# Kernel optimization log

Measured on AMD Instinct MI355X. Metric: run time of the kernel, lower is better.

## Reference

```python
import jax, jax.numpy as jnp
import numpy as np
import math

D_MODEL = 1024
NUM_HEADS = 16
D_HEAD = D_MODEL // NUM_HEADS          # 64
N_FREQ = D_HEAD // 2 + 1               # 33 rfft bins
COMPRESSION_RATIO = 0.5


def setup_inputs() -> dict:
    key = jax.random.key(0)
    k_x, k_qkv, k_out, k_b, k_m = jax.random.split(key, 5)
    B, S = 2, 2048
    x = jax.random.normal(k_x, (B, S, D_MODEL), dtype=jnp.float32)
    # Linear weights stored as [in, out] (torch Linear uses [out, in]; math identical).
    w_qkv = jax.random.normal(k_qkv, (D_MODEL, 3 * D_MODEL), dtype=jnp.float32) / math.sqrt(D_MODEL)
    w_out = jax.random.normal(k_out, (D_MODEL, D_MODEL), dtype=jnp.float32) / math.sqrt(D_MODEL)
    b_out = jax.random.normal(k_b, (D_MODEL,), dtype=jnp.float32) * 0.01
    # Learned per-frequency-bin mask logits of AdaptiveFrequencyMask(d_state=d_head).
    # Initialized around logit(compression_ratio) with small noise.
    init_logit = math.log(COMPRESSION_RATIO / (1.0 - COMPRESSION_RATIO))
    mask_logits = init_logit + 0.1 * jax.random.normal(k_m, (N_FREQ,), dtype=jnp.float32)
    return {"x": x, "w_qkv": w_qkv, "w_out": w_out, "b_out": b_out, "mask_logits": mask_logits}


def _spectral_filter(t, mask):
    # rfft over d_head dim, apply learned soft mask, inverse rfft.  t: [B,H,S,dh]
    tf = jnp.fft.rfft(t, axis=-1)          # [B,H,S,N_FREQ] complex
    tf = tf * mask                          # broadcast real mask over bins
    return jnp.fft.irfft(tf, n=t.shape[-1], axis=-1).astype(t.dtype)


def reference(x, w_qkv, w_out, b_out, mask_logits):
    B, S, D = x.shape
    H, dh = NUM_HEADS, D_HEAD
    qkv = x @ w_qkv                                         # [B,S,3D]
    q, k, v = jnp.split(qkv, 3, axis=-1)
    # [B,S,D] -> [B,H,S,dh]
    to_heads = lambda t: t.reshape(B, S, H, dh).transpose(0, 2, 1, 3)
    q, k, v = to_heads(q), to_heads(k), to_heads(v)
    mask = jax.nn.sigmoid(mask_logits)                      # [N_FREQ]
    q = _spectral_filter(q, mask)
    k = _spectral_filter(k, mask)
    scores = jnp.einsum('bhqd,bhkd->bhqk', q, k) / math.sqrt(dh)
    attn = jax.nn.softmax(scores, axis=-1)                  # dropout p=0 (eval)
    out = jnp.einsum('bhqk,bhkd->bhqd', attn, v)
    out = out.transpose(0, 2, 1, 3).reshape(B, S, D)
    return out @ w_out + b_out
```

## Files before the change

### kernel.cpp

```cpp
#include <hip/hip_runtime.h>

#define S_LEN 2048
#define NH    16
#define DH    64
#define DM    1024
#define NQKV  3072

typedef __attribute__((ext_vector_type(8))) __bf16 bf16x8;
typedef __attribute__((ext_vector_type(4))) float  f32x4;
typedef unsigned short ushort_t;

static __device__ __forceinline__ unsigned short bf16b(float f) {
  return __builtin_bit_cast(unsigned short, (__bf16)f);
}

static __device__ __forceinline__ float exp2v(float x) {
  return __builtin_amdgcn_exp2f(x);
}

static __device__ __forceinline__ bf16x8 pack8(float4 f0, float4 f1) {
  uint4 v;
  v.x = ((unsigned)bf16b(f0.y) << 16) | bf16b(f0.x);
  v.y = ((unsigned)bf16b(f0.w) << 16) | bf16b(f0.z);
  v.z = ((unsigned)bf16b(f1.y) << 16) | bf16b(f1.x);
  v.w = ((unsigned)bf16b(f1.w) << 16) | bf16b(f1.z);
  return __builtin_bit_cast(bf16x8, v);
}

static __device__ __forceinline__ void glds16(const void* g, void* l) {
  __builtin_amdgcn_global_load_lds((const __attribute__((address_space(1))) unsigned int*)g,
                                   (__attribute__((address_space(3))) unsigned int*)l, 16, 0, 0);
}

#define OFF_WT  65536ull
#define OFF_WOT 6356992ull
#define OFF_Q   8454144ull
#define OFF_K   16842752ull
#define OFF_V   25231360ull
#define OFF_AO  33619968ull

__global__ __launch_bounds__(256) void k_prep(const float* __restrict__ wqkv,
                                              const float* __restrict__ wout,
                                              const float* __restrict__ x,
                                              const float* __restrict__ logits,
                                              unsigned short* __restrict__ Wt,
                                              unsigned short* __restrict__ Wot,
                                              unsigned short* __restrict__ xb) {
  __shared__ __align__(16) char sbuf[16640];
  int bid = blockIdx.x;
  int t = threadIdx.x;

  if (bid < 256) {
    float* msk = (float*)sbuf;
    float* Kd  = (float*)(sbuf + 144);
    ushort_t (*Fb)[72] = (ushort_t(*)[72])(sbuf + 416);
    if (t < 33) msk[t] = 1.0f / (1.0f + __expf(-logits[t]));
    __syncthreads();
    if (t < 64) {
      float acc = msk[0];
      #pragma unroll
      for (int f = 1; f < 32; ++f) {
        int r = (f * t) & 63;
        acc += 2.0f * msk[f] * __cosf((float)r * (6.28318530717958647692f / 64.0f));
      }
      acc += msk[32] * ((t & 1) ? -1.0f : 1.0f);
      Kd[t] = acc * (1.0f / 64.0f);
    }
    __syncthreads();
    for (int idx = t; idx < 4096; idx += 256) {
      int j = idx >> 6, i = idx & 63;
      Fb[j][i] = bf16b(Kd[(j - i) & 63]);
    }
    __syncthreads();

    int lane = t & 63, w = t >> 6;
    int m16 = lane & 15, quad = lane >> 4;
    int kx = bid >> 5, yy = bid & 31;
    int which = yy >> 4, h = yy & 15;
    int base = which * 1024 + h * 64;

    bf16x8 af0 = *(const bf16x8*)(&Fb[w * 16 + m16][quad * 8]);
    bf16x8 af1 = *(const bf16x8*)(&Fb[w * 16 + m16][32 + quad * 8]);

    f32x4 acc[8] = {};
    #pragma unroll 2
    for (int n = 0; n < 8; ++n) {
      const float* Wg = wqkv + (size_t)(kx * 128 + n * 16 + m16) * NQKV + base + quad * 8;
      float4 a0 = *(const float4*)(Wg);
      float4 a1 = *(const float4*)(Wg + 4);
      float4 b0 = *(const float4*)(Wg + 32);
      float4 b1 = *(const float4*)(Wg + 36);
      acc[n] = __builtin_amdgcn_mfma_f32_16x16x32_bf16(af0, pack8(a0, a1), acc[n], 0, 0, 0);
      acc[n] = __builtin_amdgcn_mfma_f32_16x16x32_bf16(af1, pack8(b0, b1), acc[n], 0, 0, 0);
    }
    float sc = (which == 0) ? 0.18033688011112042f : 1.0f;
    #pragma unroll
    for (int n = 0; n < 8; ++n) {
      #pragma unroll
      for (int r = 0; r < 4; ++r) {
        int j = w * 16 + quad * 4 + r;
        Wt[(size_t)(base + j) * DM + kx * 128 + n * 16 + m16] = bf16b(acc[n][r] * sc);
      }
    }
  } else if (bid < 768) {
    float (*Ts)[65] = (float(*)[65])sbuf;
    int b1 = bid - 256;
    if (b1 < 256) {
      int kt = b1 & 15, nt = b1 >> 4;
      int cb = 2048 + nt * 64, kbase = kt * 64;
      #pragma unroll
      for (int p = 0; p < 16; ++p) {
        int kk = p * 4 + (t >> 6);
        Ts[kk][t & 63] = wqkv[(size_t)(kbase + kk) * NQKV + cb + (t & 63)];
      }
      __syncthreads();
      #pragma unroll
      for (int p = 0; p < 16; ++p) {
        int nn = p * 4 + (t >> 6);
        Wt[(size_t)(cb + nn) * DM + kbase + (t & 63)] = bf16b(Ts[t & 63][nn]);
      }
    } else {
      int b2 = b1 - 256;
      int kt = b2 & 15, nt = b2 >> 4;
      int cb = nt * 64, kbase = kt * 64;
      #pragma unroll
      for (int p = 0; p < 16; ++p) {
        int kk = p * 4 + (t >> 6);
        Ts[kk][t & 63] = wout[(size_t)(kbase + kk) * DM + cb + (t & 63)];
      }
      __syncthreads();
      #pragma unroll
      for (int p = 0; p < 16; ++p) {
        int nn = p * 4 + (t >> 6);
        Wot[(size_t)(cb + nn) * DM + kbase + (t & 63)] = bf16b(Ts[t & 63][nn]);
      }
    }
  } else {
    size_t i = ((size_t)(bid - 768) * 256 + t) * 8;
    const float4* xp = (const float4*)(x + i);
    float4 a = xp[0], b = xp[1];
    uint4 v;
    v.x = ((unsigned)bf16b(a.y) << 16) | bf16b(a.x);
    v.y = ((unsigned)bf16b(a.w) << 16) | bf16b(a.z);
    v.z = ((unsigned)bf16b(b.y) << 16) | bf16b(b.x);
    v.w = ((unsigned)bf16b(b.w) << 16) | bf16b(b.z);
    *(uint4*)(xb + i) = v;
  }
}

__device__ __forceinline__ void gemm_core_async(const unsigned short* __restrict__ A,
                                                const unsigned short* __restrict__ Bw,
                                                int bm, int bn, unsigned short* smem,
                                                f32x4 (&acc)[4][4]) {
  unsigned short* As = smem;
  unsigned short* Bs = smem + 8192;
  int t = threadIdx.x, lane = t & 63, w = t >> 6;
  int m16 = lane & 15, quad = lane >> 4;
  int wr = (w >> 1) * 64, wc = (w & 1) * 64;
  int lr = lane >> 3, lc = lane & 7;
  int gc = lc ^ lr;
  int xr = m16 & 7;
  const unsigned short* Agb = A  + (size_t)(bm * 128) * DM + gc * 8;
  const unsigned short* Bgb = Bw + (size_t)(bn * 128) * DM + gc * 8;

  for (int k0 = 0; k0 < DM; k0 += 64) {
    #pragma unroll
    for (int p = 0; p < 4; ++p) {
      int row = p * 32 + w * 8 + lr;
      glds16(Agb + (size_t)row * DM + k0, As + row * 64 + lc * 8);
      glds16(Bgb + (size_t)row * DM + k0, Bs + row * 64 + lc * 8);
    }
    __syncthreads();
    #pragma unroll
    for (int kk = 0; kk < 2; ++kk) {
      bf16x8 af[4], bfr[4];
      #pragma unroll
      for (int i = 0; i < 4; ++i)
        af[i] = *(const bf16x8*)(As + (wr + i * 16 + m16) * 64 + ((kk * 4 + quad) ^ xr) * 8);
      #pragma unroll
      for (int j = 0; j < 4; ++j)
        bfr[j] = *(const bf16x8*)(Bs + (wc + j * 16 + m16) * 64 + ((kk * 4 + quad) ^ xr) * 8);
      #pragma unroll
      for (int i = 0; i < 4; ++i)
        #pragma unroll
        for (int j = 0; j < 4; ++j)
          acc[i][j] = __builtin_amdgcn_mfma_f32_16x16x32_bf16(af[i], bfr[j], acc[i][j], 0, 0, 0);
    }
    __syncthreads();
  }
}

__global__ __launch_bounds__(256) void k_gemm_qkv(const unsigned short* __restrict__ xb,
                                                  const unsigned short* __restrict__ Bw,
                                                  unsigned short* __restrict__ Qb,
                                                  unsigned short* __restrict__ Kb,
                                                  unsigned short* __restrict__ Vt) {
  __shared__ __align__(16) unsigned short smem[18432];
  f32x4 acc[4][4] = {};
  int bn = blockIdx.x, bm = blockIdx.y;
  gemm_core_async(xb, Bw, bm, bn, smem, acc);

  int t = threadIdx.x, lane = t & 63, w = t >> 6;
  int m16 = lane & 15, quad = lane >> 4;
  int wr = (w >> 1) * 64, wc = (w & 1) * 64;
  int b = bm >> 4, srow = (bm & 15) * 128;
  int which = bn >> 3;
  ushort_t (*Tr)[130] = (ushort_t(*)[130])smem;
  if (which < 2) {
    #pragma unroll
    for (int i = 0; i < 4; ++i)
      #pragma unroll
      for (int j = 0; j < 4; ++j)
        #pragma unroll
        for (int r = 0; r < 4; ++r)
          Tr[wr + i * 16 + quad * 4 + r][wc + j * 16 + m16] = bf16b(acc[i][j][r]);
    __syncthreads();
    int row = t >> 1, half = t & 1;
    int cloc = bn * 128 + half * 64 - which * 1024;
    int h = cloc >> 6;
    unsigned short* dst = (which ? Kb : Qb) +
        ((size_t)(b * 16 + h) * 2048 + srow + row) * 64;
    #pragma unroll
    for (int p = 0; p < 8; ++p)
      *(uint4*)(dst + p * 8) = *(const uint4*)(&Tr[row][half * 64 + p * 8]);
  } else {
    #pragma unroll
    for (int i = 0; i < 4; ++i)
      #pragma unroll
      for (int j = 0; j < 4; ++j)
        #pragma unroll
        for (int r = 0; r < 4; ++r)
          Tr[wc + j * 16 + m16][wr + i * 16 + quad * 4 + r] = bf16b(acc[i][j][r]);
    __syncthreads();
    int dl = t >> 1, half = t & 1;
    int cloc = (bn - 16) * 128 + dl;
    int h = cloc >> 6, d = cloc & 63;
    unsigned short* dst = Vt + ((size_t)(b * 16 + h) * 64 + d) * 2048 + srow + half * 64;
    #pragma unroll
    for (int p = 0; p < 8; ++p)
      *(uint4*)(dst + p * 8) = *(const uint4*)(&Tr[dl][half * 64 + p * 8]);
  }
}

__global__ __launch_bounds__(512, 2) void k_attn(const unsigned short* __restrict__ Qb,
                                                 const unsigned short* __restrict__ Kb,
                                                 const unsigned short* __restrict__ Vt,
                                                 unsigned short* __restrict__ AO) {
  __shared__ __align__(16) unsigned short smem[41984];
  int t = threadIdx.x;
  int w = t >> 6, lane = t & 63;
  int m16 = lane & 15, quad = lane >> 4;
  int bid = blockIdx.x;
  int jj = bid >> 3;
  int bh = ((jj & 3) << 3) + (bid & 7);
  int qbase = (jj >> 2) * 256 + w * 32;

  const unsigned short* QpA = Qb + ((size_t)bh * S_LEN + qbase + m16) * DH + quad * 8;
  const unsigned short* QpB = QpA + 16 * DH;
  bf16x8 aq0A = *(const bf16x8*)(QpA);
  bf16x8 aq1A = *(const bf16x8*)(QpA + 32);
  bf16x8 aq0B = *(const bf16x8*)(QpB);
  bf16x8 aq1B = *(const bf16x8*)(QpB + 32);
  const unsigned short* Kbase = Kb + (size_t)bh * S_LEN * DH;
  const unsigned short* Vbase = Vt + (size_t)bh * DH * S_LEN;

  unsigned short* Pw = smem + 24576 + w * 2176;
  int xr = m16 & 7;

  int trow = t >> 3;
  int tcol = t & 7;
  int gswz = tcol ^ (trow & 7);
  const unsigned short* Kg = Kbase + (size_t)trow * 64 + gswz * 8;
  const unsigned short* Vg = Vbase + (size_t)trow * S_LEN + gswz * 8;
  unsigned short* Kl = smem + trow * 64 + tcol * 8;
  unsigned short* Vl = smem + 12288 + trow * 64 + tcol * 8;

  f32x4 oA[4] = {}, oB[4] = {};
  float lA = 0.f, lB = 0.f;
  f32x4 zero = {0.f, 0.f, 0.f, 0.f};

  glds16(Kg,        Kl);
  glds16(Vg,        Vl);
  glds16(Kg + 4096, Kl + 4096);
  glds16(Vg + 64,   Vl + 4096);

  int buf = 0, slot = 2;
  #pragma unroll 1
  for (int kt = 0; kt < S_LEN / 64; ++kt) {
    if (kt + 1 < S_LEN / 64) asm volatile("s_waitcnt vmcnt(2)" ::: "memory");
    else                     asm volatile("s_waitcnt vmcnt(0)" ::: "memory");
    __builtin_amdgcn_s_barrier();
    __builtin_amdgcn_sched_barrier(0);
    if (kt + 2 < S_LEN / 64) {
      glds16(Kg + (size_t)(kt + 2) * 4096, Kl + slot * 4096);
      glds16(Vg + (kt + 2) * 64,           Vl + slot * 4096);
    }
    unsigned short* Ksh = smem + buf * 4096;
    unsigned short* Vsh = smem + 12288 + buf * 4096;

    f32x4 stA[4], stB[4];
    __builtin_amdgcn_s_setprio(1);
    #pragma unroll
    for (int g = 0; g < 4; ++g) {
      int rk = g * 16 + m16;
      bf16x8 kf0 = *(const bf16x8*)(Ksh + rk * 64 + ((quad ^ xr) * 8));
      bf16x8 kf1 = *(const bf16x8*)(Ksh + rk * 64 + (((4 + quad) ^ xr) * 8));
      stA[g] = __builtin_amdgcn_mfma_f32_16x16x32_bf16(kf0, aq0A, zero, 0, 0, 0);
      stA[g] = __builtin_amdgcn_mfma_f32_16x16x32_bf16(kf1, aq1A, stA[g], 0, 0, 0);
      stB[g] = __builtin_amdgcn_mfma_f32_16x16x32_bf16(kf0, aq0B, zero, 0, 0, 0);
      stB[g] = __builtin_amdgcn_mfma_f32_16x16x32_bf16(kf1, aq1B, stB[g], 0, 0, 0);
    }
    __builtin_amdgcn_s_setprio(0);
    #pragma unroll
    for (int g = 0; g < 4; ++g) {
      float a0 = exp2v(stA[g][0]), a1 = exp2v(stA[g][1]);
      float a2 = exp2v(stA[g][2]), a3 = exp2v(stA[g][3]);
      lA += (a0 + a1) + (a2 + a3);
      uint2 pka;
      pka.x = ((unsigned)bf16b(a1) << 16) | bf16b(a0);
      pka.y = ((unsigned)bf16b(a3) << 16) | bf16b(a2);
      *(uint2*)(Pw + m16 * 68 + g * 16 + quad * 4) = pka;
      float b0 = exp2v(stB[g][0]), b1 = exp2v(stB[g][1]);
      float b2 = exp2v(stB[g][2]), b3 = exp2v(stB[g][3]);
      lB += (b0 + b1) + (b2 + b3);
      uint2 pkb;
      pkb.x = ((unsigned)bf16b(b1) << 16) | bf16b(b0);
      pkb.y = ((unsigned)bf16b(b3) << 16) | bf16b(b2);
      *(uint2*)(Pw + (16 + m16) * 68 + g * 16 + quad * 4) = pkb;
    }
    __builtin_amdgcn_s_setprio(1);
    #pragma unroll
    for (int c = 0; c < 2; ++c) {
      bf16x8 apA = *(const bf16x8*)(Pw + m16 * 68 + c * 32 + quad * 8);
      bf16x8 apB = *(const bf16x8*)(Pw + (16 + m16) * 68 + c * 32 + quad * 8);
      #pragma unroll
      for (int j = 0; j < 4; ++j) {
        int dv = j * 16 + m16;
        bf16x8 bv = *(const bf16x8*)(Vsh + dv * 64 + (((c * 4 + quad) ^ xr) * 8));
        oA[j] = __builtin_amdgcn_mfma_f32_16x16x32_bf16(apA, bv, oA[j], 0, 0, 0);
        oB[j] = __builtin_amdgcn_mfma_f32_16x16x32_bf16(apB, bv, oB[j], 0, 0, 0);
      }
    }
    __builtin_amdgcn_s_setprio(0);
    buf  = (buf  == 2) ? 0 : buf  + 1;
    slot = (slot == 2) ? 0 : slot + 1;
  }

  lA += __shfl_xor(lA, 16); lA += __shfl_xor(lA, 32);
  lB += __shfl_xor(lB, 16); lB += __shfl_xor(lB, 32);
  float ivA = 1.0f / lA;
  float ivB = 1.0f / lB;
  int b = bh >> 4, h = bh & 15;
  #pragma unroll
  for (int r = 0; r < 4; ++r) {
    float vA = __shfl(ivA, quad * 4 + r);
    float vB = __shfl(ivB, quad * 4 + r);
    size_t row0 = (size_t)b * S_LEN + qbase + quad * 4 + r;
    unsigned short* d0 = AO + row0 * DM + h * DH + m16;
    unsigned short* d1 = AO + (row0 + 16) * DM + h * DH + m16;
    #pragma unroll
    for (int j = 0; j < 4; ++j) {
      d0[j * 16] = bf16b(oA[j][r] * vA);
      d1[j * 16] = bf16b(oB[j][r] * vB);
    }
  }
}

__global__ __launch_bounds__(256) void k_gemm_out(const unsigned short* __restrict__ A,
                                                  const unsigned short* __restrict__ Bw,
                                                  const float* __restrict__ bias,
                                                  float* __restrict__ out) {
  __shared__ __align__(16) unsigned short smem[18432];
  f32x4 acc[4][4] = {};
  int bn = blockIdx.x, bm = blockIdx.y;
  gemm_core_async(A, Bw, bm, bn, smem, acc);

  int t = threadIdx.x, lane = t & 63, w = t >> 6;
  int m16 = lane & 15, quad = lane >> 4;
  int wr = (w >> 1) * 64, wc = (w & 1) * 64;
  #pragma unroll
  for (int i = 0; i < 4; ++i) {
    int grow = bm * 128 + wr + i * 16 + quad * 4;
    #pragma unroll
    for (int j = 0; j < 4; ++j) {
      int gc = bn * 128 + wc + j * 16 + m16;
      float bb = bias[gc];
      #pragma unroll
      for (int r = 0; r < 4; ++r)
        out[(size_t)(grow + r) * DM + gc] = acc[i][j][r] + bb;
    }
  }
}

extern "C" void kernel_launch(void* const* d_in, const int* in_sizes, int n_in,
                              void* d_out, int out_size, void* d_ws, size_t ws_size,
                              hipStream_t stream) {
  const float* x    = (const float*)d_in[0];
  const float* wqkv = (const float*)d_in[1];
  const float* wout = (const float*)d_in[2];
  const float* bout = (const float*)d_in[3];
  const float* mlog = (const float*)d_in[4];
  char* ws = (char*)d_ws;
  unsigned short* Wt  = (unsigned short*)(ws + OFF_WT);
  unsigned short* Wot = (unsigned short*)(ws + OFF_WOT);
  unsigned short* Qb  = (unsigned short*)(ws + OFF_Q);
  unsigned short* Kb  = (unsigned short*)(ws + OFF_K);
  unsigned short* Vt  = (unsigned short*)(ws + OFF_V);
  unsigned short* xb  = (unsigned short*)(ws + OFF_AO);
  unsigned short* AO  = (unsigned short*)(ws + OFF_AO);
  float* out = (float*)d_out;

  k_prep<<<dim3(2816), dim3(256), 0, stream>>>(wqkv, wout, x, mlog, Wt, Wot, xb);
  k_gemm_qkv<<<dim3(24, 32), dim3(256), 0, stream>>>(xb, Wt, Qb, Kb, Vt);
  k_attn<<<dim3(256), dim3(512), 0, stream>>>(Qb, Kb, Vt, AO);
  k_gemm_out<<<dim3(8, 32), dim3(256), 0, stream>>>(AO, Wot, bout, out);
}
```

Baseline: 218.8 us.

## Process two KV tiles per window with software-pipelined QK and PV stages

The attention loop now handles 128 keys per iteration as two 64-key tiles. The second tile's QK^T MFMAs are interleaved between the first tile's softmax and PV, and K/V loads are issued two tiles at a time into a four-slot double-buffered LDS ring, with one barrier before each refill. The P staging buffer drops the padded 68-stride layout for an XOR-swizzled 64-stride layout with two P slots per wave, and the setprio hints are removed. LDS per block grows from about 82KB to 128KB, which may limit occupancy to one block per CU despite launch_bounds(512,2).

```diff
diff --git a/kernel.cpp b/kernel.cpp
--- a/kernel.cpp
+++ b/kernel.cpp
@@ -246,7 +246,7 @@
                                                  const unsigned short* __restrict__ Kb,
                                                  const unsigned short* __restrict__ Vt,
                                                  unsigned short* __restrict__ AO) {
-  __shared__ __align__(16) unsigned short smem[41984];
+  __shared__ __align__(16) unsigned short smem[65536];
   int t = threadIdx.x;
   int w = t >> 6, lane = t & 63;
   int m16 = lane & 15, quad = lane >> 4;
@@ -264,8 +264,8 @@
   const unsigned short* Kbase = Kb + (size_t)bh * S_LEN * DH;
   const unsigned short* Vbase = Vt + (size_t)bh * DH * S_LEN;
 
-  unsigned short* Pw = smem + 24576 + w * 2176;
   int xr = m16 & 7;
+  unsigned short* Pw = smem + 32768 + w * 4096;
 
   int trow = t >> 3;
   int tcol = t & 7;
@@ -273,77 +273,122 @@
   const unsigned short* Kg = Kbase + (size_t)trow * 64 + gswz * 8;
   const unsigned short* Vg = Vbase + (size_t)trow * S_LEN + gswz * 8;
   unsigned short* Kl = smem + trow * 64 + tcol * 8;
-  unsigned short* Vl = smem + 12288 + trow * 64 + tcol * 8;
+  unsigned short* Vl = smem + 16384 + trow * 64 + tcol * 8;
 
   f32x4 oA[4] = {}, oB[4] = {};
   float lA = 0.f, lB = 0.f;
   f32x4 zero = {0.f, 0.f, 0.f, 0.f};
 
-  glds16(Kg,        Kl);
-  glds16(Vg,        Vl);
-  glds16(Kg + 4096, Kl + 4096);
-  glds16(Vg + 64,   Vl + 4096);
-
-  int buf = 0, slot = 2;
+  #pragma unroll
+  for (int tt = 0; tt < 4; ++tt) {
+    glds16(Kg + (size_t)tt * 4096, Kl + tt * 4096);
+    glds16(Vg + tt * 64,           Vl + tt * 4096);
+  }
+
   #pragma unroll 1
-  for (int kt = 0; kt < S_LEN / 64; ++kt) {
-    if (kt + 1 < S_LEN / 64) asm volatile("s_waitcnt vmcnt(2)" ::: "memory");
-    else                     asm volatile("s_waitcnt vmcnt(0)" ::: "memory");
+  for (int wnd = 0; wnd < 16; ++wnd) {
+    if (wnd < 15) asm volatile("s_waitcnt vmcnt(4)" ::: "memory");
+    else          asm volatile("s_waitcnt vmcnt(0)" ::: "memory");
     __builtin_amdgcn_s_barrier();
     __builtin_amdgcn_sched_barrier(0);
-    if (kt + 2 < S_LEN / 64) {
-      glds16(Kg + (size_t)(kt + 2) * 4096, Kl + slot * 4096);
-      glds16(Vg + (kt + 2) * 64,           Vl + slot * 4096);
-    }
-    unsigned short* Ksh = smem + buf * 4096;
-    unsigned short* Vsh = smem + 12288 + buf * 4096;
-
-    f32x4 stA[4], stB[4];
-    __builtin_amdgcn_s_setprio(1);
+    int sb = (wnd & 1) << 1;
+    const unsigned short* Ka  = smem + sb * 4096;
+    const unsigned short* Kbs = smem + (sb + 1) * 4096;
+    const unsigned short* Va  = smem + 16384 + sb * 4096;
+    const unsigned short* Vbs = smem + 16384 + (sb + 1) * 4096;
+    unsigned short* Pa = Pw;
+    unsigned short* Pb = Pw + 2048;
+
+    f32x4 saA[4], saB[4];
     #pragma unroll
     for (int g = 0; g < 4; ++g) {
       int rk = g * 16 + m16;
-      bf16x8 kf0 = *(const bf16x8*)(Ksh + rk * 64 + ((quad ^ xr) * 8));
-      bf16x8 kf1 = *(const bf16x8*)(Ksh + rk * 64 + (((4 + quad) ^ xr) * 8));
-      stA[g] = __builtin_amdgcn_mfma_f32_16x16x32_bf16(kf0, aq0A, zero, 0, 0, 0);
-      stA[g] = __builtin_amdgcn_mfma_f32_16x16x32_bf16(kf1, aq1A, stA[g], 0, 0, 0);
-      stB[g] = __builtin_amdgcn_mfma_f32_16x16x32_bf16(kf0, aq0B, zero, 0, 0, 0);
-      stB[g] = __builtin_amdgcn_mfma_f32_16x16x32_bf16(kf1, aq1B, stB[g], 0, 0, 0);
-    }
-    __builtin_amdgcn_s_setprio(0);
+      bf16x8 kf0 = *(const bf16x8*)(Ka + rk * 64 + ((quad ^ xr) * 8));
+      bf16x8 kf1 = *(const bf16x8*)(Ka + rk * 64 + (((4 + quad) ^ xr) * 8));
+      saA[g] = __builtin_amdgcn_mfma_f32_16x16x32_bf16(kf0, aq0A, zero, 0, 0, 0);
+      saA[g] = __builtin_amdgcn_mfma_f32_16x16x32_bf16(kf1, aq1A, saA[g], 0, 0, 0);
+      saB[g] = __builtin_amdgcn_mfma_f32_16x16x32_bf16(kf0, aq0B, zero, 0, 0, 0);
+      saB[g] = __builtin_amdgcn_mfma_f32_16x16x32_bf16(kf1, aq1B, saB[g], 0, 0, 0);
+    }
     #pragma unroll
     for (int g = 0; g < 4; ++g) {
-      float a0 = exp2v(stA[g][0]), a1 = exp2v(stA[g][1]);
-      float a2 = exp2v(stA[g][2]), a3 = exp2v(stA[g][3]);
+      int chw = (((2 * g + (quad >> 1)) ^ xr) << 3) + ((quad & 1) << 2);
+      float a0 = exp2v(saA[g][0]), a1 = exp2v(saA[g][1]);
+      float a2 = exp2v(saA[g][2]), a3 = exp2v(saA[g][3]);
       lA += (a0 + a1) + (a2 + a3);
       uint2 pka;
       pka.x = ((unsigned)bf16b(a1) << 16) | bf16b(a0);
       pka.y = ((unsigned)bf16b(a3) << 16) | bf16b(a2);
-      *(uint2*)(Pw + m16 * 68 + g * 16 + quad * 4) = pka;
-      float b0 = exp2v(stB[g][0]), b1 = exp2v(stB[g][1]);
-      float b2 = exp2v(stB[g][2]), b3 = exp2v(stB[g][3]);
+      *(uint2*)(Pa + m16 * 64 + chw) = pka;
+      float b0 = exp2v(saB[g][0]), b1 = exp2v(saB[g][1]);
+      float b2 = exp2v(saB[g][2]), b3 = exp2v(saB[g][3]);
       lB += (b0 + b1) + (b2 + b3);
       uint2 pkb;
       pkb.x = ((unsigned)bf16b(b1) << 16) | bf16b(b0);
       pkb.y = ((unsigned)bf16b(b3) << 16) | bf16b(b2);
-      *(uint2*)(Pw + (16 + m16) * 68 + g * 16 + quad * 4) = pkb;
-    }
-    __builtin_amdgcn_s_setprio(1);
+      *(uint2*)(Pa + (16 + m16) * 64 + chw) = pkb;
+    }
+    f32x4 sbA[4], sbB[4];
+    #pragma unroll
+    for (int g = 0; g < 4; ++g) {
+      int rk = g * 16 + m16;
+      bf16x8 kf0 = *(const bf16x8*)(Kbs + rk * 64 + ((quad ^ xr) * 8));
+      bf16x8 kf1 = *(const bf16x8*)(Kbs + rk * 64 + (((4 + quad) ^ xr) * 8));
+      sbA[g] = __builtin_amdgcn_mfma_f32_16x16x32_bf16(kf0, aq0A, zero, 0, 0, 0);
+      sbA[g] = __builtin_amdgcn_mfma_f32_16x16x32_bf16(kf1, aq1A, sbA[g], 0, 0, 0);
+      sbB[g] = __builtin_amdgcn_mfma_f32_16x16x32_bf16(kf0, aq0B, zero, 0, 0, 0);
+      sbB[g] = __builtin_amdgcn_mfma_f32_16x16x32_bf16(kf1, aq1B, sbB[g], 0, 0, 0);
+    }
     #pragma unroll
     for (int c = 0; c < 2; ++c) {
-      bf16x8 apA = *(const bf16x8*)(Pw + m16 * 68 + c * 32 + quad * 8);
-      bf16x8 apB = *(const bf16x8*)(Pw + (16 + m16) * 68 + c * 32 + quad * 8);
+      bf16x8 apA = *(const bf16x8*)(Pa + m16 * 64 + (((4 * c + quad) ^ xr) << 3));
+      bf16x8 apB = *(const bf16x8*)(Pa + (16 + m16) * 64 + (((4 * c + quad) ^ xr) << 3));
       #pragma unroll
       for (int j = 0; j < 4; ++j) {
         int dv = j * 16 + m16;
-        bf16x8 bv = *(const bf16x8*)(Vsh + dv * 64 + (((c * 4 + quad) ^ xr) * 8));
+        bf16x8 bv = *(const bf16x8*)(Va + dv * 64 + (((c * 4 + quad) ^ xr) * 8));
         oA[j] = __builtin_amdgcn_mfma_f32_16x16x32_bf16(apA, bv, oA[j], 0, 0, 0);
         oB[j] = __builtin_amdgcn_mfma_f32_16x16x32_bf16(apB, bv, oB[j], 0, 0, 0);
       }
     }
-    __builtin_amdgcn_s_setprio(0);
-    buf  = (buf  == 2) ? 0 : buf  + 1;
-    slot = (slot == 2) ? 0 : slot + 1;
+    #pragma unroll
+    for (int g = 0; g < 4; ++g) {
+      int chw = (((2 * g + (quad >> 1)) ^ xr) << 3) + ((quad & 1) << 2);
+      float a0 = exp2v(sbA[g][0]), a1 = exp2v(sbA[g][1]);
+      float a2 = exp2v(sbA[g][2]), a3 = exp2v(sbA[g][3]);
+      lA += (a0 + a1) + (a2 + a3);
+      uint2 pka;
+      pka.x = ((unsigned)bf16b(a1) << 16) | bf16b(a0);
+      pka.y = ((unsigned)bf16b(a3) << 16) | bf16b(a2);
+      *(uint2*)(Pb + m16 * 64 + chw) = pka;
+      float b0 = exp2v(sbB[g][0]), b1 = exp2v(sbB[g][1]);
+      float b2 = exp2v(sbB[g][2]), b3 = exp2v(sbB[g][3]);
+      lB += (b0 + b1) + (b2 + b3);
+      uint2 pkb;
+      pkb.x = ((unsigned)bf16b(b1) << 16) | bf16b(b0);
+      pkb.y = ((unsigned)bf16b(b3) << 16) | bf16b(b2);
+      *(uint2*)(Pb + (16 + m16) * 64 + chw) = pkb;
+    }
+    #pragma unroll
+    for (int c = 0; c < 2; ++c) {
+      bf16x8 apA = *(const bf16x8*)(Pb + m16 * 64 + (((4 * c + quad) ^ xr) << 3));
+      bf16x8 apB = *(const bf16x8*)(Pb + (16 + m16) * 64 + (((4 * c + quad) ^ xr) << 3));
+      #pragma unroll
+      for (int j = 0; j < 4; ++j) {
+        int dv = j * 16 + m16;
+        bf16x8 bv = *(const bf16x8*)(Vbs + dv * 64 + (((c * 4 + quad) ^ xr) * 8));
+        oA[j] = __builtin_amdgcn_mfma_f32_16x16x32_bf16(apA, bv, oA[j], 0, 0, 0);
+        oB[j] = __builtin_amdgcn_mfma_f32_16x16x32_bf16(apB, bv, oB[j], 0, 0, 0);
+      }
+    }
+    if (wnd < 14) {
+      __builtin_amdgcn_s_barrier();
+      int ta = 2 * wnd + 4;
+      glds16(Kg + (size_t)ta * 4096,       Kl + sb * 4096);
+      glds16(Vg + ta * 64,                 Vl + sb * 4096);
+      glds16(Kg + (size_t)(ta + 1) * 4096, Kl + (sb + 1) * 4096);
+      glds16(Vg + (ta + 1) * 64,           Vl + (sb + 1) * 4096);
+    }
   }
 
   lA += __shfl_xor(lA, 16); lA += __shfl_xor(lA, 32);
```

New measurement: 196.7 us. -10.1%, faster.
